# Performance work log

Hardware: AMD Instinct MI355X
Metric: run time of the kernel (lower is better)

## Reference

```python
import jax, jax.numpy as jnp
import numpy as np

N = 20000      # nodes
E = 640000     # edges (avg degree 32)
F = 128        # hidden_channels == num_filters
RBF = 64       # num_rbf
H = 8          # num_heads
DH = F // H    # head dim
T = 5          # number of distinct element types present in z
CUT = 5.0      # cutoff_upper (cutoff_lower = 0)


def setup_inputs() -> dict:
    key = jax.random.key(0)
    ks = jax.random.split(key, 20)
    s = 0.05
    inp = {
        "x": jax.random.normal(ks[0], (N, F), jnp.float32),
        "z": jax.random.randint(ks[1], (N,), 0, T, jnp.int32),
        "edge_index": jax.random.randint(ks[2], (2, E), 0, N, jnp.int32),
        "edge_weight": jax.random.uniform(ks[3], (E,), jnp.float32) * CUT,
        "edge_attr": jax.random.normal(ks[4], (E, RBF), jnp.float32),
        # ElemConv params
        "lin1_w": jax.random.normal(ks[5], (F, F), jnp.float32) / np.sqrt(F),
        "f_w1": jax.random.normal(ks[6], (F, RBF), jnp.float32) / np.sqrt(RBF),
        "f_b1": jnp.zeros((F,), jnp.float32),
        "f_w2": jax.random.normal(ks[7], (F, F), jnp.float32) / np.sqrt(F),
        "f_b2": jnp.zeros((F,), jnp.float32),
        # ElemAttn params
        "q_w": jax.random.normal(ks[8], (F, F), jnp.float32) / np.sqrt(F),
        "q_b": jax.random.normal(ks[9], (F,), jnp.float32) * s,
        "k_w": jax.random.normal(ks[10], (F, F), jnp.float32) / np.sqrt(F),
        "k_b": jax.random.normal(ks[11], (F,), jnp.float32) * s,
        "v_w": jax.random.normal(ks[12], (F, F), jnp.float32) / np.sqrt(F),
        "v_b": jax.random.normal(ks[13], (F,), jnp.float32) * s,
        "o1_w": jax.random.normal(ks[14], (F, F), jnp.float32) / np.sqrt(F),
        "o1_b": jax.random.normal(ks[15], (F,), jnp.float32) * s,
        "o2_w": jax.random.normal(ks[16], (F, F), jnp.float32) / np.sqrt(F),
        "o2_b": jax.random.normal(ks[17], (F,), jnp.float32) * s,
    }
    return inp


def reference(x, z, edge_index, edge_weight, edge_attr,
              lin1_w, f_w1, f_b1, f_w2, f_b2,
              q_w, q_b, k_w, k_b, v_w, v_b, o1_w, o1_b, o2_w, o2_b):
    silu = jax.nn.silu
    src, dst = edge_index[0], edge_index[1]

    # ---- ElemConv ----
    # CosineCutoff (cutoff_lower = 0)
    C = 0.5 * (jnp.cos(edge_weight * (jnp.pi / CUT)) + 1.0)
    C = C * (edge_weight < CUT).astype(x.dtype)
    # filter_net(edge_attr) * C
    W = silu(edge_attr @ f_w1.T + f_b1) @ f_w2.T + f_b2          # [E, F]
    W = W * C[:, None]
    xl = x @ lin1_w.T                                             # [N, F]
    msg = xl[src] * W                                             # [E, F]
    # aggregate by unique (z_j, dst) pair == dense [N, T] slot grid
    seg = dst * T + z[src]                                        # [E]
    y = jax.ops.segment_sum(msg, seg, num_segments=N * T).reshape(N, T, F)
    cnt = jax.ops.segment_sum(jnp.ones((E,), x.dtype), seg, num_segments=N * T)
    pm = (cnt > 0).astype(x.dtype).reshape(N, T)                  # presence mask

    # ---- ElemAttn (block-diagonal per target node over present slots) ----
    q = (y @ q_w.T + q_b).reshape(N, T, H, DH)
    k = (y @ k_w.T + k_b).reshape(N, T, H, DH)
    v = (y @ v_w.T + v_b).reshape(N, T, H, DH)
    attn = silu(jnp.einsum('nihd,njhd->nhij', q, k))              # [N, H, T, T]
    attn = attn * (pm[:, None, :, None] * pm[:, None, None, :])
    out = jnp.einsum('nhij,njhd->nihd', attn, v).reshape(N, T, F)
    out = out @ o1_w.T + o1_b                                     # [N, T, F]
    node = jnp.einsum('ntf,nt->nf', out, pm)                      # scatter-add by node
    return silu(node @ o2_w.T + o2_b)                             # [N, F]
```

## Files before the change

### kernel.cpp

```cpp
#include <hip/hip_runtime.h>

#define N_NODES 20000
#define E_EDGES 640000
#define F_DIM 128
#define RBF_DIM 64
#define T_TYPES 5
#define NSEG (N_NODES * T_TYPES)
#define EPB 128

typedef __attribute__((ext_vector_type(8))) short short8;
typedef __attribute__((ext_vector_type(4))) float f32x4;

__device__ __forceinline__ float silu_f(float x) { return x / (1.0f + __expf(-x)); }

__device__ __forceinline__ ushort f2bf(float f) {
  unsigned u = __float_as_uint(f);
  u += 0x7fffu + ((u >> 16) & 1u);
  return (ushort)(u >> 16);
}
__device__ __forceinline__ float bf2f(ushort u) {
  return __uint_as_float(((unsigned)u) << 16);
}
__device__ __forceinline__ unsigned cvt_pk(float lo, float hi) {
  unsigned r;
  asm("v_cvt_pk_bf16_f32 %0, %1, %2" : "=v"(r) : "v"(lo), "v"(hi));
  return r;
}
union S8U4 {
  short8 s;
  unsigned u[4];
};

__global__ __launch_bounds__(256) void prep_kernel(
    const float* __restrict__ w1, const float* __restrict__ w2,
    const float* __restrict__ qw, const float* __restrict__ kw,
    const float* __restrict__ vw, ushort* __restrict__ w1b,
    ushort* __restrict__ w2b, ushort* __restrict__ qwb,
    ushort* __restrict__ kwb, ushort* __restrict__ vwb) {
  int i = blockIdx.x * 256 + threadIdx.x;
  if (i < F_DIM * RBF_DIM) w1b[i] = f2bf(w1[i]);
  if (i < F_DIM * F_DIM) {
    w2b[i] = f2bf(w2[i]);
    qwb[i] = f2bf(qw[i]);
    kwb[i] = f2bf(kw[i]);
    vwb[i] = f2bf(vw[i]);
  }
}

__global__ __launch_bounds__(256) void hist_kernel(const int* __restrict__ srcp,
                                                   const int* __restrict__ dstp,
                                                   const int* __restrict__ z,
                                                   int* __restrict__ hist) {
  int e = blockIdx.x * 256 + threadIdx.x;
  int s = srcp[e];
  int seg = dstp[e] * T_TYPES + z[s];
  atomicAdd(&hist[seg], 1);
}

__global__ __launch_bounds__(256) void scan1_kernel(const int* __restrict__ hist,
                                                    int* __restrict__ offs,
                                                    int* __restrict__ bsums) {
  __shared__ int lds[256];
  int tid = threadIdx.x;
  int base = blockIdx.x * 1024 + tid * 4;
  int v[4];
  int s = 0;
#pragma unroll
  for (int i = 0; i < 4; ++i) {
    v[i] = (base + i < NSEG) ? hist[base + i] : 0;
    s += v[i];
  }
  lds[tid] = s;
  __syncthreads();
  for (int d = 1; d < 256; d <<= 1) {
    int t = (tid >= d) ? lds[tid - d] : 0;
    __syncthreads();
    lds[tid] += t;
    __syncthreads();
  }
  int excl = lds[tid] - s;
#pragma unroll
  for (int i = 0; i < 4; ++i) {
    if (base + i < NSEG) offs[base + i] = excl;
    excl += v[i];
  }
  if (tid == 255) bsums[blockIdx.x] = lds[255];
}

__global__ __launch_bounds__(128) void scan2_kernel(int* __restrict__ bsums,
                                                    int nb) {
  __shared__ int lds[128];
  int tid = threadIdx.x;
  int v = (tid < nb) ? bsums[tid] : 0;
  lds[tid] = v;
  __syncthreads();
  for (int d = 1; d < 128; d <<= 1) {
    int t = (tid >= d) ? lds[tid - d] : 0;
    __syncthreads();
    lds[tid] += t;
    __syncthreads();
  }
  if (tid < nb) bsums[tid] = lds[tid] - v;
}

__global__ __launch_bounds__(256) void scan3_kernel(const int* __restrict__ offs,
                                                    const int* __restrict__ bsums,
                                                    int* __restrict__ cursor) {
  int tid = threadIdx.x;
  int base = blockIdx.x * 1024 + tid * 4;
  int add = bsums[blockIdx.x];
#pragma unroll
  for (int i = 0; i < 4; ++i)
    if (base + i < NSEG) cursor[base + i] = offs[base + i] + add;
}

__global__ __launch_bounds__(256) void scatter_kernel(const int* __restrict__ srcp,
                                                      const int* __restrict__ dstp,
                                                      const int* __restrict__ z,
                                                      int* __restrict__ cursor,
                                                      int* __restrict__ perm) {
  int e = blockIdx.x * 256 + threadIdx.x;
  int s = srcp[e];
  int seg = dstp[e] * T_TYPES + z[s];
  int pos = atomicAdd(&cursor[seg], 1);
  perm[pos] = e;
}

__global__ __launch_bounds__(128) void lin1_kernel(const float* __restrict__ x,
                                                   const float* __restrict__ w,
                                                   ushort* __restrict__ xlb) {
  __shared__ float xs[8 * 128];
  int tid = threadIdx.x;
  int n0 = blockIdx.x * 8;
  const float4* xg = (const float4*)(x + (size_t)n0 * 128);
  float4* xs4 = (float4*)xs;
  for (int i = tid; i < 256; i += 128) xs4[i] = xg[i];
  __syncthreads();
  int f = tid;
  float acc[8] = {};
  const float4* w4 = (const float4*)(w + (size_t)f * 128);
  for (int j4 = 0; j4 < 32; ++j4) {
    float4 wv = w4[j4];
#pragma unroll
    for (int n = 0; n < 8; ++n) {
      float4 xv = xs4[n * 32 + j4];
      acc[n] += wv.x * xv.x + wv.y * xv.y + wv.z * xv.z + wv.w * xv.w;
    }
  }
  for (int n = 0; n < 8; ++n) xlb[(size_t)(n0 + n) * 128 + f] = f2bf(acc[n]);
}

__global__ __launch_bounds__(256, 4) void edge_mfma_kernel(
    const float* __restrict__ edge_attr, const int* __restrict__ srcp,
    const int* __restrict__ dstp, const float* __restrict__ ewp,
    const int* __restrict__ z, const int* __restrict__ perm,
    const ushort* __restrict__ w1b, const float* __restrict__ b1,
    const ushort* __restrict__ w2b, const float* __restrict__ b2,
    const ushort* __restrict__ xlb, float* __restrict__ y) {
  __shared__ ushort hs[128 * 136];
  __shared__ float sC[EPB];
  __shared__ int srcoff[EPB];
  __shared__ int sseg[EPB];
  __shared__ unsigned long long smask[2];

  const int tid = threadIdx.x;
  const int e0 = blockIdx.x * EPB;
  const int lane = tid & 63;
  const int w = tid >> 6;
  const int wm = w >> 1, wn = w & 1;
  const int lr = lane & 15, lh = lane >> 4;

  int prow[4];
#pragma unroll
  for (int fm = 0; fm < 4; ++fm) prow[fm] = perm[e0 + wm * 64 + fm * 16 + lr];

  float rb1[4], rb2[4];
#pragma unroll
  for (int fc = 0; fc < 4; ++fc) {
    int n = wn * 64 + fc * 16 + lr;
    rb1[fc] = b1[n];
    rb2[fc] = b2[n];
  }

  if (tid < EPB) {
    int e = perm[e0 + tid];
    int s = srcp[e];
    srcoff[tid] = s * 128;
    sseg[tid] = dstp[e] * T_TYPES + z[s];
    float wd = ewp[e];
    float c = 0.5f * (__cosf(wd * 0.6283185307179586f) + 1.0f);
    sC[tid] = (wd < 5.0f) ? c : 0.0f;
  }

  f32x4 acc[4][4] = {};
#pragma unroll
  for (int ks = 0; ks < 2; ++ks) {
    const int k0 = ks * 32;
    short8 af[4], bfr[4];
#pragma unroll
    for (int fm = 0; fm < 4; ++fm) {
      const float* ap = edge_attr + (size_t)prow[fm] * 64 + k0 + lh * 8;
      float4 a0 = *(const float4*)ap;
      float4 a1 = *(const float4*)(ap + 4);
      S8U4 t;
      t.u[0] = cvt_pk(a0.x, a0.y);
      t.u[1] = cvt_pk(a0.z, a0.w);
      t.u[2] = cvt_pk(a1.x, a1.y);
      t.u[3] = cvt_pk(a1.z, a1.w);
      af[fm] = t.s;
    }
#pragma unroll
    for (int fc = 0; fc < 4; ++fc)
      bfr[fc] = *(const short8*)(w1b + (size_t)(wn * 64 + fc * 16 + lr) * 64 +
                                 k0 + lh * 8);
#pragma unroll
    for (int fm = 0; fm < 4; ++fm)
#pragma unroll
      for (int fc = 0; fc < 4; ++fc)
        acc[fm][fc] = __builtin_amdgcn_mfma_f32_16x16x32_bf16(
            af[fm], bfr[fc], acc[fm][fc], 0, 0, 0);
  }

#pragma unroll
  for (int fm = 0; fm < 4; ++fm) {
#pragma unroll
    for (int fc = 0; fc < 4; ++fc) {
#pragma unroll
      for (int rp = 0; rp < 4; rp += 2) {
        int ml0 = wm * 64 + fm * 16 + lh * 4 + rp;
        int ml1 = ml0 + 1;
        int n = wn * 64 + fc * 16 + lr;
        float h0 = silu_f(acc[fm][fc][rp] + rb1[fc]);
        float h1 = silu_f(acc[fm][fc][rp + 1] + rb1[fc]);
        unsigned u = cvt_pk(h0, h1);
        hs[(ml0 * 256 + ((n * 2) ^ ((ml0 & 7) << 4))) >> 1] = (ushort)u;
        hs[(ml1 * 256 + ((n * 2) ^ ((ml1 & 7) << 4))) >> 1] = (ushort)(u >> 16);
      }
    }
  }
  __syncthreads();

  if (tid < EPB) {
    int head = (tid == 0) || (sseg[tid] != sseg[tid - 1]);
    unsigned long long m = __ballot(head);
    if ((tid & 63) == 0) smask[tid >> 6] = m;
  }

  f32x4 acc2[4][4] = {};
#pragma unroll
  for (int ks = 0; ks < 4; ++ks) {
    const int k0 = ks * 32;
    short8 af[4], bfr[4];
#pragma unroll
    for (int fm = 0; fm < 4; ++fm) {
      int ml = wm * 64 + fm * 16 + lr;
      int byte_in_row = (k0 * 2 + lh * 16) ^ ((ml & 7) << 4);
      af[fm] = *(const short8*)&hs[(ml * 256 + byte_in_row) >> 1];
    }
#pragma unroll
    for (int fc = 0; fc < 4; ++fc)
      bfr[fc] = *(const short8*)(w2b + (size_t)(wn * 64 + fc * 16 + lr) * 128 +
                                 k0 + lh * 8);
#pragma unroll
    for (int fm = 0; fm < 4; ++fm)
#pragma unroll
      for (int fc = 0; fc < 4; ++fc)
        acc2[fm][fc] = __builtin_amdgcn_mfma_f32_16x16x32_bf16(
            af[fm], bfr[fc], acc2[fm][fc], 0, 0, 0);
  }
  __syncthreads();

#pragma unroll
  for (int fm = 0; fm < 4; ++fm) {
#pragma unroll
    for (int rp = 0; rp < 4; rp += 2) {
      int ml0 = wm * 64 + fm * 16 + lh * 4 + rp;
      float c0 = sC[ml0], c1 = sC[ml0 + 1];
#pragma unroll
      for (int fc = 0; fc < 4; ++fc) {
        int n = wn * 64 + fc * 16 + lr;
        float v0 = (acc2[fm][fc][rp] + rb2[fc]) * c0;
        float v1 = (acc2[fm][fc][rp + 1] + rb2[fc]) * c1;
        *(unsigned*)&hs[n * 136 + ml0] = cvt_pk(v0, v1);
      }
    }
  }
  __syncthreads();

  {
    int cp = tid & 63;
    int q = tid >> 6;
    int rbase = q * 32;
    int c0 = cp * 2;
    unsigned mm = (unsigned)(smask[q >> 1] >> ((q & 1) * 32));
    float a0 = 0.0f, a1 = 0.0f;
    int cur = sseg[rbase];
    bool first = true;
#pragma unroll
    for (int it = 0; it < 4; ++it) {
      int r0 = rbase + it * 8;
      short8 m0 = *(const short8*)&hs[c0 * 136 + r0];
      short8 m1 = *(const short8*)&hs[(c0 + 1) * 136 + r0];
      unsigned xv[8];
#pragma unroll
      for (int j = 0; j < 8; ++j)
        xv[j] = *(const unsigned*)&xlb[(size_t)srcoff[r0 + j] + c0];
#pragma unroll
      for (int j = 0; j < 8; ++j) {
        int rr = it * 8 + j;
        if (rr && ((mm >> rr) & 1u)) {
          float* yp = &y[(size_t)cur * 128 + c0];
          if (first) {
            atomicAdd(yp, a0);
            atomicAdd(yp + 1, a1);
            first = false;
          } else {
            yp[0] = a0;
            yp[1] = a1;
          }
          a0 = a1 = 0.0f;
          cur = sseg[r0 + j];
        }
        a0 += bf2f((ushort)m0[j]) * bf2f((ushort)xv[j]);
        a1 += bf2f((ushort)m1[j]) * bf2f((ushort)(xv[j] >> 16));
      }
    }
    float* yp = &y[(size_t)cur * 128 + c0];
    atomicAdd(yp, a0);
    atomicAdd(yp + 1, a1);
  }
}

#define QS 136
#define NB 16
__global__ __launch_bounds__(256) void attn_fused_kernel(
    const float* __restrict__ y, const int* __restrict__ hist,
    const ushort* __restrict__ qwb, const ushort* __restrict__ kwb,
    const ushort* __restrict__ vwb, const float* __restrict__ qb,
    const float* __restrict__ kb, const float* __restrict__ vb,
    float* __restrict__ sout) {
  __shared__ ushort bufA[80 * QS];
  __shared__ ushort bufB[80 * QS];
  __shared__ float aa[NB * 8 * 5];
  __shared__ float pmv[80];
  __shared__ float sxb[3][128];

  const int tid = threadIdx.x;
  const int n0 = blockIdx.x * NB;
  const int row0 = n0 * T_TYPES;
  const int lane = tid & 63;
  const int w = tid >> 6;
  const int lr = lane & 15, lh = lane >> 4;

  if (tid < 128) {
    sxb[0][tid] = qb[tid];
    sxb[1][tid] = kb[tid];
    sxb[2][tid] = vb[tid];
  }
  if (tid < 80) pmv[tid] = (hist[(size_t)row0 + tid] > 0) ? 1.0f : 0.0f;

  short8 A[4][5];
#pragma unroll
  for (int ksi = 0; ksi < 4; ++ksi) {
#pragma unroll
    for (int fm = 0; fm < 5; ++fm) {
      const float* ap =
          y + (size_t)(row0 + fm * 16 + lr) * 128 + ksi * 32 + lh * 8;
      float4 a0 = *(const float4*)ap;
      float4 a1 = *(const float4*)(ap + 4);
      S8U4 t;
      t.u[0] = cvt_pk(a0.x, a0.y);
      t.u[1] = cvt_pk(a0.z, a0.w);
      t.u[2] = cvt_pk(a1.x, a1.y);
      t.u[3] = cvt_pk(a1.z, a1.w);
      A[ksi][fm] = t.s;
    }
  }
  __syncthreads();

  auto do_proj = [&](const ushort* __restrict__ Wb, const float* bias_row,
                     ushort* __restrict__ dst) {
    f32x4 acc[5][2] = {};
#pragma unroll
    for (int ksi = 0; ksi < 4; ++ksi) {
      short8 B[2];
#pragma unroll
      for (int fc = 0; fc < 2; ++fc)
        B[fc] = *(const short8*)(Wb + (size_t)(w * 32 + fc * 16 + lr) * 128 +
                                 ksi * 32 + lh * 8);
#pragma unroll
      for (int fm = 0; fm < 5; ++fm)
#pragma unroll
        for (int fc = 0; fc < 2; ++fc)
          acc[fm][fc] = __builtin_amdgcn_mfma_f32_16x16x32_bf16(
              A[ksi][fm], B[fc], acc[fm][fc], 0, 0, 0);
    }
#pragma unroll
    for (int fm = 0; fm < 5; ++fm)
#pragma unroll
      for (int fc = 0; fc < 2; ++fc)
#pragma unroll
        for (int rp = 0; rp < 4; rp += 2) {
          int rrow = fm * 16 + lh * 4 + rp;
          int col = w * 32 + fc * 16 + lr;
          float v0 = acc[fm][fc][rp] + bias_row[col];
          float v1 = acc[fm][fc][rp + 1] + bias_row[col];
          unsigned u = cvt_pk(v0, v1);
          dst[rrow * QS + col] = (ushort)u;
          dst[(rrow + 1) * QS + col] = (ushort)(u >> 16);
        }
  };

  do_proj(qwb, sxb[0], bufA);
  do_proj(kwb, sxb[1], bufB);
  __syncthreads();

  if (tid < NB * 8) {
    int n = tid >> 3, h = tid & 7;
    float kv[5][16];
#pragma unroll
    for (int j = 0; j < 5; ++j) {
      short8 v0 = *(const short8*)&bufB[(n * 5 + j) * QS + h * 16];
      short8 v1 = *(const short8*)&bufB[(n * 5 + j) * QS + h * 16 + 8];
#pragma unroll
      for (int d = 0; d < 8; ++d) {
        kv[j][d] = bf2f((ushort)v0[d]);
        kv[j][d + 8] = bf2f((ushort)v1[d]);
      }
    }
    float a[5] = {};
    for (int i = 0; i < 5; ++i) {
      float qv[16];
      short8 q0 = *(const short8*)&bufA[(n * 5 + i) * QS + h * 16];
      short8 q1 = *(const short8*)&bufA[(n * 5 + i) * QS + h * 16 + 8];
#pragma unroll
      for (int d = 0; d < 8; ++d) {
        qv[d] = bf2f((ushort)q0[d]);
        qv[d + 8] = bf2f((ushort)q1[d]);
      }
      float pmi = pmv[n * 5 + i];
#pragma unroll
      for (int j = 0; j < 5; ++j) {
        float dd = 0.0f;
#pragma unroll
        for (int d = 0; d < 16; ++d) dd += qv[d] * kv[j][d];
        a[j] += pmi * silu_f(dd);
      }
    }
#pragma unroll
    for (int j = 0; j < 5; ++j) aa[(n * 8 + h) * 5 + j] = a[j] * pmv[n * 5 + j];
  }
  __syncthreads();

  do_proj(vwb, sxb[2], bufA);
  __syncthreads();

  {
    int n = tid >> 4;
    int o = tid & 15;
    int f0 = o * 8;
    int h = f0 >> 4;
    float acc8[8] = {};
#pragma unroll
    for (int j = 0; j < 5; ++j) {
      float a = aa[(n * 8 + h) * 5 + j];
      short8 vv8 = *(const short8*)&bufA[(n * 5 + j) * QS + f0];
#pragma unroll
      for (int d = 0; d < 8; ++d) acc8[d] += a * bf2f((ushort)vv8[d]);
    }
    float* op = sout + (size_t)(n0 + n) * 128 + f0;
    *(float4*)op = make_float4(acc8[0], acc8[1], acc8[2], acc8[3]);
    *(float4*)(op + 4) = make_float4(acc8[4], acc8[5], acc8[6], acc8[7]);
  }
}

__global__ __launch_bounds__(128) void out_kernel(
    const float* __restrict__ sbufg, const int* __restrict__ hist,
    const float* __restrict__ o1w, const float* __restrict__ o1b,
    const float* __restrict__ o2w, const float* __restrict__ o2b,
    float* __restrict__ outp) {
  __shared__ float sb[8 * 128];
  __shared__ float t1[8 * 128];
  __shared__ float npm[8];
  int tid = threadIdx.x;
  int n0 = blockIdx.x * 8;
  const float4* sg4 = (const float4*)(sbufg + (size_t)n0 * 128);
  float4* sb4 = (float4*)sb;
  for (int i = tid; i < 256; i += 128) sb4[i] = sg4[i];
  if (tid < 8) {
    float s = 0.0f;
    for (int t = 0; t < T_TYPES; ++t)
      s += (hist[(size_t)(n0 + tid) * T_TYPES + t] > 0) ? 1.0f : 0.0f;
    npm[tid] = s;
  }
  __syncthreads();
  int f = tid;
  {
    const float4* wg = (const float4*)(o1w + (size_t)f * 128);
    float acc[8] = {};
    for (int j4 = 0; j4 < 32; ++j4) {
      float4 wv = wg[j4];
#pragma unroll
      for (int n = 0; n < 8; ++n) {
        float4 sv = sb4[n * 32 + j4];
        acc[n] += wv.x * sv.x + wv.y * sv.y + wv.z * sv.z + wv.w * sv.w;
      }
    }
    float bb = o1b[f];
    for (int n = 0; n < 8; ++n) t1[n * 128 + f] = acc[n] + npm[n] * bb;
  }
  __syncthreads();
  {
    const float4* wg = (const float4*)(o2w + (size_t)f * 128);
    const float4* t14 = (const float4*)t1;
    float acc[8] = {};
    for (int j4 = 0; j4 < 32; ++j4) {
      float4 wv = wg[j4];
#pragma unroll
      for (int n = 0; n < 8; ++n) {
        float4 tv = t14[n * 32 + j4];
        acc[n] += wv.x * tv.x + wv.y * tv.y + wv.z * tv.z + wv.w * tv.w;
      }
    }
    float bb = o2b[f];
    for (int n = 0; n < 8; ++n) outp[(size_t)(n0 + n) * 128 + f] = silu_f(acc[n] + bb);
  }
}

extern "C" void kernel_launch(void* const* d_in, const int* in_sizes, int n_in,
                              void* d_out, int out_size, void* d_ws, size_t ws_size,
                              hipStream_t stream) {
  const float* x = (const float*)d_in[0];
  const int* z = (const int*)d_in[1];
  const int* ei = (const int*)d_in[2];
  const float* ew = (const float*)d_in[3];
  const float* ea = (const float*)d_in[4];
  const float* lin1_w = (const float*)d_in[5];
  const float* fw1 = (const float*)d_in[6];
  const float* fb1 = (const float*)d_in[7];
  const float* fw2 = (const float*)d_in[8];
  const float* fb2 = (const float*)d_in[9];
  const float* qw = (const float*)d_in[10];
  const float* qb = (const float*)d_in[11];
  const float* kw = (const float*)d_in[12];
  const float* kb = (const float*)d_in[13];
  const float* vw = (const float*)d_in[14];
  const float* vb = (const float*)d_in[15];
  const float* o1w = (const float*)d_in[16];
  const float* o1b = (const float*)d_in[17];
  const float* o2w = (const float*)d_in[18];
  const float* o2b = (const float*)d_in[19];
  float* outp = (float*)d_out;
  float* ws = (float*)d_ws;

  float* sbuf = ws;
  float* y = sbuf + (size_t)N_NODES * F_DIM;
  ushort* xlb = (ushort*)(y + (size_t)NSEG * F_DIM);
  ushort* w1b = xlb + (size_t)N_NODES * F_DIM;
  ushort* w2b = w1b + F_DIM * RBF_DIM;
  ushort* qwb = w2b + F_DIM * F_DIM;
  ushort* kwb = qwb + F_DIM * F_DIM;
  ushort* vwb = kwb + F_DIM * F_DIM;
  int* hist = (int*)(vwb + F_DIM * F_DIM);
  int* offs = hist + NSEG;
  int* cursor = offs + NSEG;
  int* bsums = cursor + NSEG;
  int* perm = bsums + 128;

  const int* srcp = ei;
  const int* dstp = ei + E_EDGES;
  const int NB_SCAN = (NSEG + 1023) / 1024;

  hipMemsetAsync(y, 0, (size_t)NSEG * F_DIM * sizeof(float), stream);
  hipMemsetAsync(hist, 0, (size_t)NSEG * sizeof(int), stream);

  prep_kernel<<<64, 256, 0, stream>>>(fw1, fw2, qw, kw, vw, w1b, w2b, qwb, kwb, vwb);
  hist_kernel<<<E_EDGES / 256, 256, 0, stream>>>(srcp, dstp, z, hist);
  scan1_kernel<<<NB_SCAN, 256, 0, stream>>>(hist, offs, bsums);
  scan2_kernel<<<1, 128, 0, stream>>>(bsums, NB_SCAN);
  scan3_kernel<<<NB_SCAN, 256, 0, stream>>>(offs, bsums, cursor);
  scatter_kernel<<<E_EDGES / 256, 256, 0, stream>>>(srcp, dstp, z, cursor, perm);
  lin1_kernel<<<N_NODES / 8, 128, 0, stream>>>(x, lin1_w, xlb);
  edge_mfma_kernel<<<E_EDGES / EPB, 256, 0, stream>>>(ea, srcp, dstp, ew, z, perm,
                                                      w1b, fb1, w2b, fb2, xlb, y);
  attn_fused_kernel<<<N_NODES / NB, 256, 0, stream>>>(y, hist, qwb, kwb, vwb, qb,
                                                      kb, vb, sbuf);
  out_kernel<<<N_NODES / 8, 128, 0, stream>>>(sbuf, hist, o1w, o1b, o2w, o2b, outp);
}
```

Measured before the change: 359.1 us.

## Fuse output projections into attention kernel and replace scatter atomics with hist ranks

Merges the o1/o2 output-projection kernel into the attention kernel, keeping the per-node attention result in shared memory instead of writing it to a global buffer and reading it back. The histogram kernel now records each edge's rank within its segment, so the scatter step places edges at offset+rank without a second round of atomics or a cursor copy. The attention score loop is also split across all 256 threads (two query groups per node/head) rather than half the block. The cost is more shared-memory reuse and register pressure in the fused kernel, plus an extra rank array in global memory.

```diff
diff --git a/kernel.cpp b/kernel.cpp
--- a/kernel.cpp
+++ b/kernel.cpp
@@ -47,14 +47,13 @@
   }
 }
 
-__global__ __launch_bounds__(256) void hist_kernel(const int* __restrict__ srcp,
-                                                   const int* __restrict__ dstp,
-                                                   const int* __restrict__ z,
-                                                   int* __restrict__ hist) {
+__global__ __launch_bounds__(256) void hist_rank_kernel(
+    const int* __restrict__ srcp, const int* __restrict__ dstp,
+    const int* __restrict__ z, int* __restrict__ hist, int* __restrict__ rnk) {
   int e = blockIdx.x * 256 + threadIdx.x;
   int s = srcp[e];
   int seg = dstp[e] * T_TYPES + z[s];
-  atomicAdd(&hist[seg], 1);
+  rnk[e] = atomicAdd(&hist[seg], 1);
 }
 
 __global__ __launch_bounds__(256) void scan1_kernel(const int* __restrict__ hist,
@@ -103,27 +102,24 @@
   if (tid < nb) bsums[tid] = lds[tid] - v;
 }
 
-__global__ __launch_bounds__(256) void scan3_kernel(const int* __restrict__ offs,
-                                                    const int* __restrict__ bsums,
-                                                    int* __restrict__ cursor) {
+__global__ __launch_bounds__(256) void scan3_kernel(int* __restrict__ offs,
+                                                    const int* __restrict__ bsums) {
   int tid = threadIdx.x;
   int base = blockIdx.x * 1024 + tid * 4;
   int add = bsums[blockIdx.x];
 #pragma unroll
   for (int i = 0; i < 4; ++i)
-    if (base + i < NSEG) cursor[base + i] = offs[base + i] + add;
-}
-
-__global__ __launch_bounds__(256) void scatter_kernel(const int* __restrict__ srcp,
-                                                      const int* __restrict__ dstp,
-                                                      const int* __restrict__ z,
-                                                      int* __restrict__ cursor,
-                                                      int* __restrict__ perm) {
+    if (base + i < NSEG) offs[base + i] += add;
+}
+
+__global__ __launch_bounds__(256) void scatter_kernel(
+    const int* __restrict__ srcp, const int* __restrict__ dstp,
+    const int* __restrict__ z, const int* __restrict__ offs,
+    const int* __restrict__ rnk, int* __restrict__ perm) {
   int e = blockIdx.x * 256 + threadIdx.x;
   int s = srcp[e];
   int seg = dstp[e] * T_TYPES + z[s];
-  int pos = atomicAdd(&cursor[seg], 1);
-  perm[pos] = e;
+  perm[offs[seg] + rnk[e]] = e;
 }
 
 __global__ __launch_bounds__(128) void lin1_kernel(const float* __restrict__ x,
@@ -333,16 +329,19 @@
 
 #define QS 136
 #define NB 16
-__global__ __launch_bounds__(256) void attn_fused_kernel(
+__global__ __launch_bounds__(256) void attn_out_kernel(
     const float* __restrict__ y, const int* __restrict__ hist,
     const ushort* __restrict__ qwb, const ushort* __restrict__ kwb,
     const ushort* __restrict__ vwb, const float* __restrict__ qb,
     const float* __restrict__ kb, const float* __restrict__ vb,
-    float* __restrict__ sout) {
+    const float* __restrict__ o1w, const float* __restrict__ o1b,
+    const float* __restrict__ o2w, const float* __restrict__ o2b,
+    float* __restrict__ outp) {
   __shared__ ushort bufA[80 * QS];
   __shared__ ushort bufB[80 * QS];
-  __shared__ float aa[NB * 8 * 5];
+  __shared__ float aap[NB * 8 * 2 * 5];
   __shared__ float pmv[80];
+  __shared__ float snpm[NB];
   __shared__ float sxb[3][128];
 
   const int tid = threadIdx.x;
@@ -377,6 +376,12 @@
     }
   }
   __syncthreads();
+  if (tid < NB) {
+    float s = 0.0f;
+#pragma unroll
+    for (int t = 0; t < 5; ++t) s += pmv[tid * 5 + t];
+    snpm[tid] = s;
+  }
 
   auto do_proj = [&](const ushort* __restrict__ Wb, const float* bias_row,
                      ushort* __restrict__ dst) {
@@ -415,8 +420,10 @@
   do_proj(kwb, sxb[1], bufB);
   __syncthreads();
 
-  if (tid < NB * 8) {
-    int n = tid >> 3, h = tid & 7;
+  {
+    int n = tid >> 4, h = (tid >> 1) & 7, g = tid & 1;
+    int i0 = g ? 3 : 0;
+    int cnt = g ? 2 : 3;
     float kv[5][16];
 #pragma unroll
     for (int j = 0; j < 5; ++j) {
@@ -429,7 +436,8 @@
       }
     }
     float a[5] = {};
-    for (int i = 0; i < 5; ++i) {
+    for (int ii = 0; ii < cnt; ++ii) {
+      int i = i0 + ii;
       float qv[16];
       short8 q0 = *(const short8*)&bufA[(n * 5 + i) * QS + h * 16];
       short8 q1 = *(const short8*)&bufA[(n * 5 + i) * QS + h * 16 + 8];
@@ -448,13 +456,14 @@
       }
     }
 #pragma unroll
-    for (int j = 0; j < 5; ++j) aa[(n * 8 + h) * 5 + j] = a[j] * pmv[n * 5 + j];
+    for (int j = 0; j < 5; ++j) aap[((n * 8 + h) * 2 + g) * 5 + j] = a[j];
   }
   __syncthreads();
 
   do_proj(vwb, sxb[2], bufA);
   __syncthreads();
 
+  float* sf = (float*)bufB;
   {
     int n = tid >> 4;
     int o = tid & 15;
@@ -463,67 +472,61 @@
     float acc8[8] = {};
 #pragma unroll
     for (int j = 0; j < 5; ++j) {
-      float a = aa[(n * 8 + h) * 5 + j];
+      float a = (aap[((n * 8 + h) * 2 + 0) * 5 + j] +
+                 aap[((n * 8 + h) * 2 + 1) * 5 + j]) *
+                pmv[n * 5 + j];
       short8 vv8 = *(const short8*)&bufA[(n * 5 + j) * QS + f0];
 #pragma unroll
       for (int d = 0; d < 8; ++d) acc8[d] += a * bf2f((ushort)vv8[d]);
     }
-    float* op = sout + (size_t)(n0 + n) * 128 + f0;
+    float* op = sf + n * 128 + f0;
     *(float4*)op = make_float4(acc8[0], acc8[1], acc8[2], acc8[3]);
     *(float4*)(op + 4) = make_float4(acc8[4], acc8[5], acc8[6], acc8[7]);
   }
-}
-
-__global__ __launch_bounds__(128) void out_kernel(
-    const float* __restrict__ sbufg, const int* __restrict__ hist,
-    const float* __restrict__ o1w, const float* __restrict__ o1b,
-    const float* __restrict__ o2w, const float* __restrict__ o2b,
-    float* __restrict__ outp) {
-  __shared__ float sb[8 * 128];
-  __shared__ float t1[8 * 128];
-  __shared__ float npm[8];
-  int tid = threadIdx.x;
-  int n0 = blockIdx.x * 8;
-  const float4* sg4 = (const float4*)(sbufg + (size_t)n0 * 128);
-  float4* sb4 = (float4*)sb;
-  for (int i = tid; i < 256; i += 128) sb4[i] = sg4[i];
-  if (tid < 8) {
-    float s = 0.0f;
-    for (int t = 0; t < T_TYPES; ++t)
-      s += (hist[(size_t)(n0 + tid) * T_TYPES + t] > 0) ? 1.0f : 0.0f;
-    npm[tid] = s;
-  }
-  __syncthreads();
-  int f = tid;
+  __syncthreads();
+
+  float* t1f = (float*)bufA;
   {
+    int f = tid & 127, half = tid >> 7;
     const float4* wg = (const float4*)(o1w + (size_t)f * 128);
+    const float4* s4 = (const float4*)sf;
     float acc[8] = {};
     for (int j4 = 0; j4 < 32; ++j4) {
       float4 wv = wg[j4];
 #pragma unroll
-      for (int n = 0; n < 8; ++n) {
-        float4 sv = sb4[n * 32 + j4];
-        acc[n] += wv.x * sv.x + wv.y * sv.y + wv.z * sv.z + wv.w * sv.w;
+      for (int nn = 0; nn < 8; ++nn) {
+        float4 sv = s4[(half * 8 + nn) * 32 + j4];
+        acc[nn] += wv.x * sv.x + wv.y * sv.y + wv.z * sv.z + wv.w * sv.w;
       }
     }
     float bb = o1b[f];
-    for (int n = 0; n < 8; ++n) t1[n * 128 + f] = acc[n] + npm[n] * bb;
-  }
-  __syncthreads();
+#pragma unroll
+    for (int nn = 0; nn < 8; ++nn) {
+      int n = half * 8 + nn;
+      t1f[n * 128 + f] = acc[nn] + snpm[n] * bb;
+    }
+  }
+  __syncthreads();
+
   {
+    int f = tid & 127, half = tid >> 7;
     const float4* wg = (const float4*)(o2w + (size_t)f * 128);
-    const float4* t14 = (const float4*)t1;
+    const float4* t4 = (const float4*)t1f;
     float acc[8] = {};
     for (int j4 = 0; j4 < 32; ++j4) {
       float4 wv = wg[j4];
 #pragma unroll
-      for (int n = 0; n < 8; ++n) {
-        float4 tv = t14[n * 32 + j4];
-        acc[n] += wv.x * tv.x + wv.y * tv.y + wv.z * tv.z + wv.w * tv.w;
+      for (int nn = 0; nn < 8; ++nn) {
+        float4 tv = t4[(half * 8 + nn) * 32 + j4];
+        acc[nn] += wv.x * tv.x + wv.y * tv.y + wv.z * tv.z + wv.w * tv.w;
       }
     }
     float bb = o2b[f];
-    for (int n = 0; n < 8; ++n) outp[(size_t)(n0 + n) * 128 + f] = silu_f(acc[n] + bb);
+#pragma unroll
+    for (int nn = 0; nn < 8; ++nn) {
+      int n = half * 8 + nn;
+      outp[(size_t)(n0 + n) * 128 + f] = silu_f(acc[nn] + bb);
+    }
   }
 }
 
@@ -553,8 +556,7 @@
   float* outp = (float*)d_out;
   float* ws = (float*)d_ws;
 
-  float* sbuf = ws;
-  float* y = sbuf + (size_t)N_NODES * F_DIM;
+  float* y = ws;
   ushort* xlb = (ushort*)(y + (size_t)NSEG * F_DIM);
   ushort* w1b = xlb + (size_t)N_NODES * F_DIM;
   ushort* w2b = w1b + F_DIM * RBF_DIM;
@@ -563,9 +565,9 @@
   ushort* vwb = kwb + F_DIM * F_DIM;
   int* hist = (int*)(vwb + F_DIM * F_DIM);
   int* offs = hist + NSEG;
-  int* cursor = offs + NSEG;
-  int* bsums = cursor + NSEG;
-  int* perm = bsums + 128;
+  int* bsums = offs + NSEG;
+  int* rnk = bsums + 128;
+  int* perm = rnk + E_EDGES;
 
   const int* srcp = ei;
   const int* dstp = ei + E_EDGES;
@@ -575,15 +577,14 @@
   hipMemsetAsync(hist, 0, (size_t)NSEG * sizeof(int), stream);
 
   prep_kernel<<<64, 256, 0, stream>>>(fw1, fw2, qw, kw, vw, w1b, w2b, qwb, kwb, vwb);
-  hist_kernel<<<E_EDGES / 256, 256, 0, stream>>>(srcp, dstp, z, hist);
+  hist_rank_kernel<<<E_EDGES / 256, 256, 0, stream>>>(srcp, dstp, z, hist, rnk);
   scan1_kernel<<<NB_SCAN, 256, 0, stream>>>(hist, offs, bsums);
   scan2_kernel<<<1, 128, 0, stream>>>(bsums, NB_SCAN);
-  scan3_kernel<<<NB_SCAN, 256, 0, stream>>>(offs, bsums, cursor);
-  scatter_kernel<<<E_EDGES / 256, 256, 0, stream>>>(srcp, dstp, z, cursor, perm);
+  scan3_kernel<<<NB_SCAN, 256, 0, stream>>>(offs, bsums);
+  scatter_kernel<<<E_EDGES / 256, 256, 0, stream>>>(srcp, dstp, z, offs, rnk, perm);
   lin1_kernel<<<N_NODES / 8, 128, 0, stream>>>(x, lin1_w, xlb);
   edge_mfma_kernel<<<E_EDGES / EPB, 256, 0, stream>>>(ea, srcp, dstp, ew, z, perm,
                                                       w1b, fb1, w2b, fb2, xlb, y);
-  attn_fused_kernel<<<N_NODES / NB, 256, 0, stream>>>(y, hist, qwb, kwb, vwb, qb,
-                                                      kb, vb, sbuf);
-  out_kernel<<<N_NODES / 8, 128, 0, stream>>>(sbuf, hist, o1w, o1b, o2w, o2b, outp);
-}
+  attn_out_kernel<<<N_NODES / NB, 256, 0, stream>>>(y, hist, qwb, kwb, vwb, qb, kb,
+                                                    vb, o1w, o1b, o2w, o2b, outp);
+}
```

Measured after the change: 339.1 us. -5.6%, faster.
